# Kernel optimization log

Measured on AMD Instinct MI355X. Metric: run time of the kernel, lower is better.

## Reference

```python
import jax, jax.numpy as jnp
import numpy as np

B, S, DIM = 2, 2048, 2048
H, DK, DR, DC, DCP, DV = 16, 128, 64, 512, 1024, 128


def setup_inputs() -> dict:
    key = jax.random.key(0)
    ks = jax.random.split(key, 8)
    s = 0.02  # weight init scale
    return {
        "x": jax.random.normal(ks[0], (B, S, DIM), jnp.float32),
        "W_c": jax.random.normal(ks[1], (DIM, DC), jnp.float32) * s,
        "W_c_prime": jax.random.normal(ks[2], (DIM, DCP), jnp.float32) * s,
        "W_qc": jax.random.normal(ks[3], (H, DCP, DK), jnp.float32) * s,
        "W_qr": jax.random.normal(ks[4], (H, DCP, DR), jnp.float32) * s,
        "W_kc": jax.random.normal(ks[5], (H, DC, DK), jnp.float32) * s,
        "W_kr": jax.random.normal(ks[6], (DIM, DR), jnp.float32) * s,
        "W_v": jax.random.normal(ks[7], (H, DC, DV), jnp.float32) * s,
    }


def reference(x, W_c, W_c_prime, W_qc, W_qr, W_kc, W_kr, W_v):
    # Latent compressions
    c = x @ W_c                 # [B,S,DC]  compressed KV latent
    cp = x @ W_c_prime          # [B,S,DCP] compressed Q latent
    # Per-head projections, vectorized over heads
    q_c = jnp.einsum('bsc,hck->bhsk', cp, W_qc)   # [B,H,S,DK]
    q_r = jnp.einsum('bsc,hcr->bhsr', cp, W_qr)   # [B,H,S,DR]
    k_c = jnp.einsum('bsc,hck->bhsk', c, W_kc)    # [B,H,S,DK]
    k_r = x @ W_kr                                 # [B,S,DR] shared across heads
    q = jnp.concatenate([q_c, q_r], axis=-1)                               # [B,H,S,DK+DR]
    k = jnp.concatenate([k_c, jnp.broadcast_to(k_r[:, None], (B, H, S, DR))], axis=-1)
    scale = 1.0 / np.sqrt(DK + DR)
    scores = jnp.einsum('bhsd,bhtd->bhst', q, k) * scale                   # [B,H,S,S]
    causal = jnp.tril(jnp.ones((S, S), dtype=bool))
    scores = jnp.where(causal, scores, -jnp.inf)
    probs = jax.nn.softmax(scores.astype(jnp.float32), axis=-1).astype(q.dtype)
    v = jnp.einsum('bsc,hcv->bhsv', c, W_v)                                # [B,H,S,DV]
    out = jnp.einsum('bhst,bhtv->bhsv', probs, v)                          # [B,H,S,DV]
    return out.transpose(0, 2, 1, 3).reshape(B, S, H * DV)                 # concat heads
```

## Files before the change

kernel.cpp:

```cpp
#include <hip/hip_runtime.h>
#include <stdint.h>

typedef __bf16 bf16;
typedef __bf16 bfx8 __attribute__((ext_vector_type(8)));
typedef __bf16 bfx4 __attribute__((ext_vector_type(4)));
typedef float floatx4 __attribute__((ext_vector_type(4)));

#define B_ 2
#define S_ 2048
#define DIM_ 2048
#define H_ 16
#define DK_ 128
#define DR_ 64
#define DC_ 512
#define DCP_ 1024
#define DV_ 128
#define DQK_ 192

#define MASK_VAL (-30000.0f)
#define C1_ 0.10411754f

__global__ void k_prep(
    const float* __restrict__ x, bf16* __restrict__ xb,
    const float* __restrict__ W_c, const float* __restrict__ W_cp,
    const float* __restrict__ W_qc, const float* __restrict__ W_qr,
    const float* __restrict__ W_kc, const float* __restrict__ W_kr,
    const float* __restrict__ W_v,
    bf16* __restrict__ Wt_c, bf16* __restrict__ Wt_cp,
    bf16* __restrict__ Wt_qc, bf16* __restrict__ Wt_qr,
    bf16* __restrict__ Wt_kc, bf16* __restrict__ Wt_kr,
    bf16* __restrict__ Wt_v) {
    __shared__ float tile[32][33];
    int bid0 = blockIdx.x;
    if (bid0 < 4096) {
        size_t i = ((size_t)bid0 * 256 + threadIdx.x) * 8;
        float4 a = *(const float4*)(x + i);
        float4 b = *(const float4*)(x + i + 4);
        bfx8 r;
        r[0] = (bf16)a.x; r[1] = (bf16)a.y; r[2] = (bf16)a.z; r[3] = (bf16)a.w;
        r[4] = (bf16)b.x; r[5] = (bf16)b.y; r[6] = (bf16)b.z; r[7] = (bf16)b.w;
        *(bfx8*)(xb + i) = r;
        return;
    }
    int bid = bid0 - 4096;
    const float* in; bf16* out; int K, N, lx, ly, local;
    if (bid < 1024)      { in = W_c;  out = Wt_c;  K = 2048; N = 512;  lx = 4; ly = 6; local = bid; }
    else if (bid < 3072) { in = W_cp; out = Wt_cp; K = 2048; N = 1024; lx = 5; ly = 6; local = bid - 1024; }
    else if (bid < 5120) { in = W_qc; out = Wt_qc; K = 1024; N = 128;  lx = 2; ly = 5; local = bid - 3072; }
    else if (bid < 6144) { in = W_qr; out = Wt_qr; K = 1024; N = 64;   lx = 1; ly = 5; local = bid - 5120; }
    else if (bid < 7168) { in = W_kc; out = Wt_kc; K = 512;  N = 128;  lx = 2; ly = 4; local = bid - 6144; }
    else if (bid < 7296) { in = W_kr; out = Wt_kr; K = 2048; N = 64;   lx = 1; ly = 6; local = bid - 7168; }
    else                 { in = W_v;  out = Wt_v;  K = 512;  N = 128;  lx = 2; ly = 4; local = bid - 7296; }
    int n0 = (local & ((1 << lx) - 1)) << 5;
    int k0 = ((local >> lx) & ((1 << ly) - 1)) << 5;
    int h  = local >> (lx + ly);
    const float* ip = in + (size_t)h * K * N;
    bf16* op = out + (size_t)h * K * N;
    int tx = threadIdx.x & 31, ty = threadIdx.x >> 5;
#pragma unroll
    for (int i = 0; i < 32; i += 8)
        tile[ty + i][tx] = ip[(size_t)(k0 + ty + i) * N + (n0 + tx)];
    __syncthreads();
#pragma unroll
    for (int i = 0; i < 32; i += 8)
        op[(size_t)(n0 + ty + i) * K + (k0 + tx)] = (bf16)tile[tx][ty + i];
}

__device__ __forceinline__ void gld16(const bf16* g, bf16* l) {
    __builtin_amdgcn_global_load_lds(
        (const __attribute__((address_space(1))) void*)g,
        (__attribute__((address_space(3))) void*)l, 16, 0, 0);
}

__device__ __forceinline__ bfx8 frag_ld(const bf16* lds, int row, int quad) {
    int pb = quad ^ ((row >> 1) & 3);
    return *(const bfx8*)(lds + row * 32 + pb * 8);
}

#define SLICE_ 4096

__device__ __forceinline__ void gemm_core(const bf16* __restrict__ A,
                                          const bf16* __restrict__ Bt,
                                          int K, int rowlimB,
                                          floatx4 acc[4][4],
                                          bf16* A_lds, bf16* B_lds) {
    int tid = threadIdx.x, wave = tid >> 6, lane = tid & 63;
    int l15 = lane & 15, quad = lane >> 4;
    int wm = (wave & 1) * 64, wn = (wave >> 1) * 64;
    int ch0 = wave * 2, ch1 = wave * 2 + 1;
    int r0 = ch0 * 16 + (lane >> 2), r1 = ch1 * 16 + (lane >> 2);
    int kb0 = (lane & 3) ^ ((r0 >> 1) & 3), kb1 = (lane & 3) ^ ((r1 >> 1) & 3);
    int rb0 = r0 <= rowlimB ? r0 : rowlimB;
    int rb1 = r1 <= rowlimB ? r1 : rowlimB;
    const bf16* a0 = A + (size_t)r0 * K + kb0 * 8;
    const bf16* a1 = A + (size_t)r1 * K + kb1 * 8;
    const bf16* b0 = Bt + (size_t)rb0 * K + kb0 * 8;
    const bf16* b1 = Bt + (size_t)rb1 * K + kb1 * 8;
    bf16* da0 = A_lds + ch0 * 512;
    bf16* da1 = A_lds + ch1 * 512;
    bf16* db0 = B_lds + ch0 * 512;
    bf16* db1 = B_lds + ch1 * 512;
    for (int k0 = 0; k0 < K; k0 += 64) {
        __syncthreads();
        gld16(a0 + k0, da0);
        gld16(a1 + k0, da1);
        gld16(b0 + k0, db0);
        gld16(b1 + k0, db1);
        gld16(a0 + k0 + 32, da0 + SLICE_);
        gld16(a1 + k0 + 32, da1 + SLICE_);
        gld16(b0 + k0 + 32, db0 + SLICE_);
        gld16(b1 + k0 + 32, db1 + SLICE_);
        __syncthreads();
#pragma unroll
        for (int sl = 0; sl < 2; ++sl) {
            const bf16* As = A_lds + sl * SLICE_;
            const bf16* Bs = B_lds + sl * SLICE_;
            bfx8 a[4], b[4];
#pragma unroll
            for (int t = 0; t < 4; ++t) a[t] = frag_ld(As, wm + t * 16 + l15, quad);
#pragma unroll
            for (int t = 0; t < 4; ++t) b[t] = frag_ld(Bs, wn + t * 16 + l15, quad);
#pragma unroll
            for (int mt = 0; mt < 4; ++mt)
#pragma unroll
                for (int nt = 0; nt < 4; ++nt)
                    acc[mt][nt] = __builtin_amdgcn_mfma_f32_16x16x32_bf16(
                        a[mt], b[nt], acc[mt][nt], 0, 0, 0);
        }
    }
}

__global__ __launch_bounds__(256, 3) void k_gemm1(
    const bf16* __restrict__ xb, const bf16* __restrict__ Wt_c,
    const bf16* __restrict__ Wt_cp, const bf16* __restrict__ Wt_kr,
    bf16* __restrict__ c_ws, bf16* __restrict__ cp_ws, bf16* __restrict__ kr_ws) {
    __shared__ __attribute__((aligned(16))) bf16 A_lds[2 * SLICE_];
    __shared__ __attribute__((aligned(16))) bf16 B_lds[2 * SLICE_];
    int hw = blockIdx.x + 13 * blockIdx.y;
    int virt = (hw & 7) * 52 + (hw >> 3);
    int bx = virt % 13, by = virt / 13;
    const bf16* Bt; bf16* outp; int ldc, col0, rowlim;
    if (bx < 4)       { Bt = Wt_c  + (size_t)bx * 128 * DIM_;       outp = c_ws;  ldc = DC_;  col0 = bx * 128;       rowlim = 127; }
    else if (bx < 12) { Bt = Wt_cp + (size_t)(bx - 4) * 128 * DIM_; outp = cp_ws; ldc = DCP_; col0 = (bx - 4) * 128; rowlim = 127; }
    else              { Bt = Wt_kr;                                  outp = kr_ws; ldc = DR_;  col0 = 0;              rowlim = 63;  }
    floatx4 acc[4][4];
#pragma unroll
    for (int i = 0; i < 4; ++i)
#pragma unroll
        for (int j = 0; j < 4; ++j) acc[i][j] = (floatx4){0.f, 0.f, 0.f, 0.f};
    gemm_core(xb + (size_t)by * 128 * DIM_, Bt, DIM_, rowlim, acc, A_lds, B_lds);
    int tid = threadIdx.x, wave = tid >> 6, lane = tid & 63;
    int l15 = lane & 15, quad = lane >> 4;
    int wm = (wave & 1) * 64, wn = (wave >> 1) * 64;
#pragma unroll
    for (int mt = 0; mt < 4; ++mt)
#pragma unroll
        for (int nt = 0; nt < 4; ++nt) {
            int n = wn + nt * 16 + l15;
            if (n > rowlim) continue;
#pragma unroll
            for (int r = 0; r < 4; ++r) {
                int m = by * 128 + wm + mt * 16 + quad * 4 + r;
                outp[(size_t)m * ldc + col0 + n] = (bf16)acc[mt][nt][r];
            }
        }
}

__global__ __launch_bounds__(256, 3) void k_gemm23(
    const bf16* __restrict__ cp_ws, const bf16* __restrict__ c_ws,
    const bf16* __restrict__ Wt_qc, const bf16* __restrict__ Wt_qr,
    const bf16* __restrict__ Wt_kc, const bf16* __restrict__ Wt_v,
    bf16* __restrict__ q_ws, bf16* __restrict__ kc_ws, bf16* __restrict__ vt_ws) {
    __shared__ __attribute__((aligned(16))) bf16 A_lds[2 * SLICE_];
    __shared__ __attribute__((aligned(16))) bf16 B_lds[2 * SLICE_];
    int hw = blockIdx.x;
    int c = hw & 7, idx = hw >> 3;
    int tid = threadIdx.x, wave = tid >> 6, lane = tid & 63;
    int l15 = lane & 15, quad = lane >> 4;
    int wm = (wave & 1) * 64, wn = (wave >> 1) * 64;
    floatx4 acc[4][4];
#pragma unroll
    for (int i = 0; i < 4; ++i)
#pragma unroll
        for (int j = 0; j < 4; ++j) acc[i][j] = (floatx4){0.f, 0.f, 0.f, 0.f};
    if (idx < 96) {
        int virt = c * 96 + idx;
        int bx = virt % 3, by = (virt / 3) & 31, hz = c;
        const bf16* Bt;
        if (bx < 2) Bt = Wt_qc + (size_t)(hz * 2 + bx) * DK_ * DCP_;
        else        Bt = Wt_qr + (size_t)hz * 128 * DCP_;
        gemm_core(cp_ws + (size_t)by * 128 * DCP_, Bt, DCP_, 127, acc, A_lds, B_lds);
#pragma unroll
        for (int mt = 0; mt < 4; ++mt)
#pragma unroll
            for (int nt = 0; nt < 4; ++nt) {
                int n = wn + nt * 16 + l15;
                int h, col;
                if (bx < 2) { h = hz * 2 + bx;        col = n; }
                else        { h = hz * 2 + (n >> 6);  col = 128 + (n & 63); }
#pragma unroll
                for (int r = 0; r < 4; ++r) {
                    int m = by * 128 + wm + mt * 16 + quad * 4 + r;
                    int b = m >> 11, s = m & 2047;
                    q_ws[(((size_t)b * H_ + h) * S_ + s) * DQK_ + col] =
                        (bf16)(acc[mt][nt][r] * C1_);
                }
            }
    } else {
        int v2 = c * 128 + (idx - 96);
        int bx = v2 & 1, by = (v2 >> 1) & 31, h = v2 >> 6;
        const bf16* Bt = (bx == 0) ? (Wt_kc + (size_t)h * DK_ * DC_)
                                   : (Wt_v  + (size_t)h * DV_ * DC_);
        gemm_core(c_ws + (size_t)by * 128 * DC_, Bt, DC_, 127, acc, A_lds, B_lds);
#pragma unroll
        for (int mt = 0; mt < 4; ++mt)
#pragma unroll
            for (int nt = 0; nt < 4; ++nt) {
                int n = wn + nt * 16 + l15;
                if (bx == 0) {
#pragma unroll
                    for (int r = 0; r < 4; ++r) {
                        int m = by * 128 + wm + mt * 16 + quad * 4 + r;
                        int b = m >> 11, s = m & 2047;
                        kc_ws[(((size_t)b * H_ + h) * S_ + s) * DK_ + n] = (bf16)acc[mt][nt][r];
                    }
                } else {
                    int m0 = by * 128 + wm + mt * 16 + quad * 4;
                    int b = m0 >> 11, s = m0 & 2047;
                    bfx4 pack;
#pragma unroll
                    for (int r = 0; r < 4; ++r) pack[r] = (bf16)acc[mt][nt][r];
                    *(bfx4*)(&vt_ws[(((size_t)b * H_ + h) * DV_ + n) * S_ + s]) = pack;
                }
            }
    }
}

__global__ __launch_bounds__(256, 2) void k_attn(
    const bf16* __restrict__ q_ws, const bf16* __restrict__ kc_ws,
    const bf16* __restrict__ kr_ws, const bf16* __restrict__ vt_ws,
    float* __restrict__ out) {
    __shared__ __attribute__((aligned(16))) bf16 K_lds[6 * 2048];
    __shared__ __attribute__((aligned(16))) bf16 V_lds[2 * 4096];
    __shared__ __attribute__((aligned(16))) bf16 P_lds[2 * 2048];
    int hw = blockIdx.x + 16 * blockIdx.y;
    int virt = (hw & 7) * 64 + (hw >> 3);
    int p = virt & 15;
    int bh = virt >> 4, b = bh >> 4, h = bh & 15;
    int tid = threadIdx.x, wave = tid >> 6, lane = tid & 63;
    int l15 = lane & 15, quad = lane >> 4;

    bf16 ov = (bf16)(l15 == 0 ? 1.f : 0.f);
    bfx8 ones8 = {ov, ov, ov, ov, ov, ov, ov, ov};

    int rowk = tid >> 2;
    int kb   = (tid & 3) ^ ((tid >> 3) & 3);
    const bf16* kcp[4]; const bf16* krp[2]; const bf16* vp[4];
#pragma unroll
    for (int j = 0; j < 4; ++j)
        kcp[j] = kc_ws + ((size_t)bh * S_ + rowk) * DK_ + j * 32 + kb * 8;
#pragma unroll
    for (int j = 0; j < 2; ++j)
        krp[j] = kr_ws + ((size_t)b * S_ + rowk) * DR_ + j * 32 + kb * 8;
#pragma unroll
    for (int j = 0; j < 4; ++j)
        vp[j] = vt_ws + ((size_t)bh * DV_ + (j & 1) * 64 + rowk) * S_ + (j >> 1) * 32 + kb * 8;
    bf16* kdst = K_lds + (size_t)tid * 8;
    bf16* vdst = V_lds + (size_t)tid * 8;

    for (int ph = 0; ph < 2; ++ph) {
        int qt = ph ? p : 31 - p;
        int q0 = qt * 64, ntiles = qt + 1;

        const bf16* qrow = q_ws + ((size_t)bh * S_ + q0 + wave * 16 + l15) * DQK_;
        bfx8 qf[6];
#pragma unroll
        for (int ks = 0; ks < 6; ++ks)
            qf[ks] = *(const bfx8*)(qrow + ks * 32 + quad * 8);

        floatx4 o_acc[9];
#pragma unroll
        for (int vt = 0; vt < 9; ++vt) o_acc[vt] = (floatx4){0.f, 0.f, 0.f, 0.f};

        bfx8 pk[4], pr[2], pv[4];
#pragma unroll
        for (int j = 0; j < 4; ++j) pk[j] = *(const bfx8*)(kcp[j]);
#pragma unroll
        for (int j = 0; j < 2; ++j) pr[j] = *(const bfx8*)(krp[j]);
#pragma unroll
        for (int j = 0; j < 4; ++j) pv[j] = *(const bfx8*)(vp[j]);

        for (int t = 0; t < ntiles; ++t) {
            __syncthreads();
#pragma unroll
            for (int j = 0; j < 4; ++j) *(bfx8*)(kdst + j * 2048) = pk[j];
#pragma unroll
            for (int j = 0; j < 2; ++j) *(bfx8*)(kdst + (4 + j) * 2048) = pr[j];
#pragma unroll
            for (int j = 0; j < 4; ++j) *(bfx8*)(vdst + j * 2048) = pv[j];
            __syncthreads();
            if (t + 1 < ntiles) {
                size_t kv1 = (size_t)(t + 1) * 64;
#pragma unroll
                for (int j = 0; j < 4; ++j) pk[j] = *(const bfx8*)(kcp[j] + kv1 * DK_);
#pragma unroll
                for (int j = 0; j < 2; ++j) pr[j] = *(const bfx8*)(krp[j] + kv1 * DR_);
#pragma unroll
                for (int j = 0; j < 4; ++j) pv[j] = *(const bfx8*)(vp[j] + kv1);
            }
            floatx4 sc[4];
#pragma unroll
            for (int nt = 0; nt < 4; ++nt) sc[nt] = (floatx4){0.f, 0.f, 0.f, 0.f};
            __builtin_amdgcn_s_setprio(1);
#pragma unroll
            for (int ks = 0; ks < 6; ++ks)
#pragma unroll
                for (int nt = 0; nt < 4; ++nt) {
                    bfx8 kf = frag_ld(K_lds + ks * 2048, nt * 16 + l15, quad);
                    sc[nt] = __builtin_amdgcn_mfma_f32_16x16x32_bf16(qf[ks], kf, sc[nt], 0, 0, 0);
                }
            __builtin_amdgcn_s_setprio(0);
            if (t == ntiles - 1) {
                int kv0 = t * 64;
#pragma unroll
                for (int nt = 0; nt < 4; ++nt)
#pragma unroll
                    for (int r = 0; r < 4; ++r) {
                        int n_g = kv0 + nt * 16 + l15;
                        int q_g = q0 + wave * 16 + quad * 4 + r;
                        if (n_g > q_g) sc[nt][r] = MASK_VAL;
                    }
            }
#pragma unroll
            for (int nt = 0; nt < 4; ++nt)
#pragma unroll
                for (int r = 0; r < 4; ++r) {
                    int prow = wave * 16 + quad * 4 + r;
                    int pcol = nt * 16 + l15;
                    P_lds[(nt >> 1) * 2048 + prow * 32 +
                          ((((pcol >> 3) & 3) ^ ((prow >> 1) & 3)) * 8) + (pcol & 7)] =
                        (bf16)exp2f(sc[nt][r]);
                }
            __builtin_amdgcn_s_setprio(1);
#pragma unroll
            for (int ks2 = 0; ks2 < 2; ++ks2) {
                bfx8 pf = frag_ld(P_lds + ks2 * 2048, wave * 16 + l15, quad);
#pragma unroll
                for (int vt = 0; vt < 8; ++vt) {
                    bfx8 vf = frag_ld(V_lds + ks2 * 4096, vt * 16 + l15, quad);
                    o_acc[vt] = __builtin_amdgcn_mfma_f32_16x16x32_bf16(pf, vf, o_acc[vt], 0, 0, 0);
                }
                o_acc[8] = __builtin_amdgcn_mfma_f32_16x16x32_bf16(pf, ones8, o_acc[8], 0, 0, 0);
            }
            __builtin_amdgcn_s_setprio(0);
        }
        float rinv[4];
#pragma unroll
        for (int r = 0; r < 4; ++r)
            rinv[r] = 1.f / __shfl(o_acc[8][r], lane & 48);
#pragma unroll
        for (int vt = 0; vt < 8; ++vt)
#pragma unroll
            for (int r = 0; r < 4; ++r) {
                int s = q0 + wave * 16 + quad * 4 + r;
                int v = vt * 16 + l15;
                out[((size_t)b * S_ + s) * (H_ * DV_) + h * DV_ + v] = o_acc[vt][r] * rinv[r];
            }
    }
}

extern "C" void kernel_launch(void* const* d_in, const int* in_sizes, int n_in,
                              void* d_out, int out_size, void* d_ws, size_t ws_size,
                              hipStream_t stream) {
    const float* x    = (const float*)d_in[0];
    const float* W_c  = (const float*)d_in[1];
    const float* W_cp = (const float*)d_in[2];
    const float* W_qc = (const float*)d_in[3];
    const float* W_qr = (const float*)d_in[4];
    const float* W_kc = (const float*)d_in[5];
    const float* W_kr = (const float*)d_in[6];
    const float* W_v  = (const float*)d_in[7];
    float* out = (float*)d_out;

    bf16* c_ws  = (bf16*)d_out;
    bf16* cp_ws = c_ws + (size_t)B_ * S_ * DC_;
    bf16* xb    = cp_ws + (size_t)B_ * S_ * DCP_;

    char* ws = (char*)d_ws;
    size_t off = 0;
    auto alloc = [&](size_t elems) { bf16* p = (bf16*)(ws + off); off += elems * sizeof(bf16); return p; };
    bf16* Wt_c  = alloc((size_t)DIM_ * DC_);
    bf16* Wt_cp = alloc((size_t)DIM_ * DCP_);
    bf16* Wt_qc = alloc((size_t)H_ * DCP_ * DK_);
    bf16* Wt_qr = alloc((size_t)H_ * DCP_ * DR_);
    bf16* Wt_kc = alloc((size_t)H_ * DC_ * DK_);
    bf16* Wt_kr = alloc((size_t)DIM_ * DR_);
    bf16* Wt_v  = alloc((size_t)H_ * DC_ * DV_);
    bf16* kr_ws = alloc((size_t)B_ * S_ * DR_);
    bf16* q_ws  = alloc((size_t)B_ * H_ * S_ * DQK_);
    bf16* kc_ws = alloc((size_t)B_ * H_ * S_ * DK_);
    bf16* vt_ws = alloc((size_t)B_ * H_ * DV_ * S_);

    k_prep<<<dim3(12416), 256, 0, stream>>>(
        x, xb, W_c, W_cp, W_qc, W_qr, W_kc, W_kr, W_v,
        Wt_c, Wt_cp, Wt_qc, Wt_qr, Wt_kc, Wt_kr, Wt_v);

    k_gemm1<<<dim3(13, 32), 256, 0, stream>>>(xb, Wt_c, Wt_cp, Wt_kr, c_ws, cp_ws, kr_ws);
    k_gemm23<<<dim3(1792), 256, 0, stream>>>(cp_ws, c_ws, Wt_qc, Wt_qr, Wt_kc, Wt_v,
                                             q_ws, kc_ws, vt_ws);
    k_attn<<<dim3(16, B_ * H_), 256, 0, stream>>>(q_ws, kc_ws, kr_ws, vt_ws, out);
}
```

Measured before the change: 269.4 us.

## Double attention query tile per block and vectorize weight transpose kernel

The attention kernel now processes 128 query rows per block, each wave handling two 16-row tiles, so every K/V tile loaded into LDS feeds twice as many MFMAs. The grid halves to 256 blocks, and launch bounds drop to one block per SM to give room for the doubled accumulators. The aim is to halve K/V global and LDS traffic per output row, at the cost of lower occupancy and fewer blocks to balance across CUs. The weight transpose in the prep kernel is also rewritten to use 64x32 tiles with float4 loads and bf16x4 stores, cutting its block count and instruction overhead.

New measurement: 302.0 us. +12.1%, slower.

```diff
diff --git a/kernel.cpp b/kernel.cpp
--- a/kernel.cpp
+++ b/kernel.cpp
@@ -30,7 +30,7 @@
     bf16* __restrict__ Wt_qc, bf16* __restrict__ Wt_qr,
     bf16* __restrict__ Wt_kc, bf16* __restrict__ Wt_kr,
     bf16* __restrict__ Wt_v) {
-    __shared__ float tile[32][33];
+    __shared__ float tile[64][33];
     int bid0 = blockIdx.x;
     if (bid0 < 4096) {
         size_t i = ((size_t)bid0 * 256 + threadIdx.x) * 8;
@@ -44,26 +44,33 @@
     }
     int bid = bid0 - 4096;
     const float* in; bf16* out; int K, N, lx, ly, local;
-    if (bid < 1024)      { in = W_c;  out = Wt_c;  K = 2048; N = 512;  lx = 4; ly = 6; local = bid; }
-    else if (bid < 3072) { in = W_cp; out = Wt_cp; K = 2048; N = 1024; lx = 5; ly = 6; local = bid - 1024; }
-    else if (bid < 5120) { in = W_qc; out = Wt_qc; K = 1024; N = 128;  lx = 2; ly = 5; local = bid - 3072; }
-    else if (bid < 6144) { in = W_qr; out = Wt_qr; K = 1024; N = 64;   lx = 1; ly = 5; local = bid - 5120; }
-    else if (bid < 7168) { in = W_kc; out = Wt_kc; K = 512;  N = 128;  lx = 2; ly = 4; local = bid - 6144; }
-    else if (bid < 7296) { in = W_kr; out = Wt_kr; K = 2048; N = 64;   lx = 1; ly = 6; local = bid - 7168; }
-    else                 { in = W_v;  out = Wt_v;  K = 512;  N = 128;  lx = 2; ly = 4; local = bid - 7296; }
+    if (bid < 512)       { in = W_c;  out = Wt_c;  K = 2048; N = 512;  lx = 4; ly = 5; local = bid; }
+    else if (bid < 1536) { in = W_cp; out = Wt_cp; K = 2048; N = 1024; lx = 5; ly = 5; local = bid - 512; }
+    else if (bid < 2560) { in = W_qc; out = Wt_qc; K = 1024; N = 128;  lx = 2; ly = 4; local = bid - 1536; }
+    else if (bid < 3072) { in = W_qr; out = Wt_qr; K = 1024; N = 64;   lx = 1; ly = 4; local = bid - 2560; }
+    else if (bid < 3584) { in = W_kc; out = Wt_kc; K = 512;  N = 128;  lx = 2; ly = 3; local = bid - 3072; }
+    else if (bid < 3648) { in = W_kr; out = Wt_kr; K = 2048; N = 64;   lx = 1; ly = 5; local = bid - 3584; }
+    else                 { in = W_v;  out = Wt_v;  K = 512;  N = 128;  lx = 2; ly = 3; local = bid - 3648; }
     int n0 = (local & ((1 << lx) - 1)) << 5;
-    int k0 = ((local >> lx) & ((1 << ly) - 1)) << 5;
+    int k0 = ((local >> lx) & ((1 << ly) - 1)) << 6;
     int h  = local >> (lx + ly);
     const float* ip = in + (size_t)h * K * N;
     bf16* op = out + (size_t)h * K * N;
-    int tx = threadIdx.x & 31, ty = threadIdx.x >> 5;
-#pragma unroll
-    for (int i = 0; i < 32; i += 8)
-        tile[ty + i][tx] = ip[(size_t)(k0 + ty + i) * N + (n0 + tx)];
+    int t = threadIdx.x;
+    int kr = t >> 3, nc = (t & 7) * 4;
+#pragma unroll
+    for (int i = 0; i < 2; ++i)
+        *(float4*)(&tile[kr + i * 32][nc]) =
+            *(const float4*)(ip + (size_t)(k0 + kr + i * 32) * N + n0 + nc);
     __syncthreads();
-#pragma unroll
-    for (int i = 0; i < 32; i += 8)
-        op[(size_t)(n0 + ty + i) * K + (k0 + tx)] = (bf16)tile[tx][ty + i];
+    int nr = t >> 4, kc = (t & 15) * 4;
+#pragma unroll
+    for (int i = 0; i < 2; ++i) {
+        bfx4 w;
+#pragma unroll
+        for (int c = 0; c < 4; ++c) w[c] = (bf16)tile[kc + c][nr + i * 16];
+        *(bfx4*)(op + (size_t)(n0 + nr + i * 16) * K + k0 + kc) = w;
+    }
 }
 
 __device__ __forceinline__ void gld16(const bf16* g, bf16* l) {
@@ -236,17 +243,17 @@
     }
 }
 
-__global__ __launch_bounds__(256, 2) void k_attn(
+__global__ __launch_bounds__(256, 1) void k_attn(
     const bf16* __restrict__ q_ws, const bf16* __restrict__ kc_ws,
     const bf16* __restrict__ kr_ws, const bf16* __restrict__ vt_ws,
     float* __restrict__ out) {
     __shared__ __attribute__((aligned(16))) bf16 K_lds[6 * 2048];
     __shared__ __attribute__((aligned(16))) bf16 V_lds[2 * 4096];
-    __shared__ __attribute__((aligned(16))) bf16 P_lds[2 * 2048];
-    int hw = blockIdx.x + 16 * blockIdx.y;
-    int virt = (hw & 7) * 64 + (hw >> 3);
-    int p = virt & 15;
-    int bh = virt >> 4, b = bh >> 4, h = bh & 15;
+    __shared__ __attribute__((aligned(16))) bf16 P_lds[2 * 4096];
+    int hw = blockIdx.x + 8 * blockIdx.y;
+    int virt = (hw & 7) * 32 + (hw >> 3);
+    int p = virt & 7;
+    int bh = virt >> 3, b = bh >> 4, h = bh & 15;
     int tid = threadIdx.x, wave = tid >> 6, lane = tid & 63;
     int l15 = lane & 15, quad = lane >> 4;
 
@@ -269,18 +276,24 @@
     bf16* vdst = V_lds + (size_t)tid * 8;
 
     for (int ph = 0; ph < 2; ++ph) {
-        int qt = ph ? p : 31 - p;
-        int q0 = qt * 64, ntiles = qt + 1;
-
-        const bf16* qrow = q_ws + ((size_t)bh * S_ + q0 + wave * 16 + l15) * DQK_;
-        bfx8 qf[6];
-#pragma unroll
-        for (int ks = 0; ks < 6; ++ks)
-            qf[ks] = *(const bfx8*)(qrow + ks * 32 + quad * 8);
-
-        floatx4 o_acc[9];
-#pragma unroll
-        for (int vt = 0; vt < 9; ++vt) o_acc[vt] = (floatx4){0.f, 0.f, 0.f, 0.f};
+        int qt = ph ? p : 15 - p;
+        int q0 = qt * 128, ntiles = 2 * qt + 2;
+
+        bfx8 qf[2][6];
+#pragma unroll
+        for (int rt = 0; rt < 2; ++rt) {
+            const bf16* qrow =
+                q_ws + ((size_t)bh * S_ + q0 + wave * 32 + rt * 16 + l15) * DQK_;
+#pragma unroll
+            for (int ks = 0; ks < 6; ++ks)
+                qf[rt][ks] = *(const bfx8*)(qrow + ks * 32 + quad * 8);
+        }
+
+        floatx4 o_acc[2][9];
+#pragma unroll
+        for (int rt = 0; rt < 2; ++rt)
+#pragma unroll
+            for (int vt = 0; vt < 9; ++vt) o_acc[rt][vt] = (floatx4){0.f, 0.f, 0.f, 0.f};
 
         bfx8 pk[4], pr[2], pv[4];
 #pragma unroll
@@ -308,64 +321,78 @@
 #pragma unroll
                 for (int j = 0; j < 4; ++j) pv[j] = *(const bfx8*)(vp[j] + kv1);
             }
-            floatx4 sc[4];
-#pragma unroll
-            for (int nt = 0; nt < 4; ++nt) sc[nt] = (floatx4){0.f, 0.f, 0.f, 0.f};
+            floatx4 sc[2][4];
+#pragma unroll
+            for (int rt = 0; rt < 2; ++rt)
+#pragma unroll
+                for (int nt = 0; nt < 4; ++nt) sc[rt][nt] = (floatx4){0.f, 0.f, 0.f, 0.f};
             __builtin_amdgcn_s_setprio(1);
 #pragma unroll
             for (int ks = 0; ks < 6; ++ks)
 #pragma unroll
                 for (int nt = 0; nt < 4; ++nt) {
                     bfx8 kf = frag_ld(K_lds + ks * 2048, nt * 16 + l15, quad);
-                    sc[nt] = __builtin_amdgcn_mfma_f32_16x16x32_bf16(qf[ks], kf, sc[nt], 0, 0, 0);
+                    sc[0][nt] = __builtin_amdgcn_mfma_f32_16x16x32_bf16(qf[0][ks], kf, sc[0][nt], 0, 0, 0);
+                    sc[1][nt] = __builtin_amdgcn_mfma_f32_16x16x32_bf16(qf[1][ks], kf, sc[1][nt], 0, 0, 0);
                 }
             __builtin_amdgcn_s_setprio(0);
-            if (t == ntiles - 1) {
+            if (t >= ntiles - 2) {
                 int kv0 = t * 64;
 #pragma unroll
+                for (int rt = 0; rt < 2; ++rt)
+#pragma unroll
+                    for (int nt = 0; nt < 4; ++nt)
+#pragma unroll
+                        for (int r = 0; r < 4; ++r) {
+                            int n_g = kv0 + nt * 16 + l15;
+                            int q_g = q0 + wave * 32 + rt * 16 + quad * 4 + r;
+                            if (n_g > q_g) sc[rt][nt][r] = MASK_VAL;
+                        }
+            }
+#pragma unroll
+            for (int rt = 0; rt < 2; ++rt)
+#pragma unroll
                 for (int nt = 0; nt < 4; ++nt)
 #pragma unroll
                     for (int r = 0; r < 4; ++r) {
-                        int n_g = kv0 + nt * 16 + l15;
-                        int q_g = q0 + wave * 16 + quad * 4 + r;
-                        if (n_g > q_g) sc[nt][r] = MASK_VAL;
+                        int prow = wave * 32 + rt * 16 + quad * 4 + r;
+                        int pcol = nt * 16 + l15;
+                        P_lds[(nt >> 1) * 4096 + prow * 32 +
+                              ((((pcol >> 3) & 3) ^ ((prow >> 1) & 3)) * 8) + (pcol & 7)] =
+                            (bf16)exp2f(sc[rt][nt][r]);
                     }
-            }
-#pragma unroll
-            for (int nt = 0; nt < 4; ++nt)
-#pragma unroll
-                for (int r = 0; r < 4; ++r) {
-                    int prow = wave * 16 + quad * 4 + r;
-                    int pcol = nt * 16 + l15;
-                    P_lds[(nt >> 1) * 2048 + prow * 32 +
-                          ((((pcol >> 3) & 3) ^ ((prow >> 1) & 3)) * 8) + (pcol & 7)] =
-                        (bf16)exp2f(sc[nt][r]);
-                }
             __builtin_amdgcn_s_setprio(1);
 #pragma unroll
             for (int ks2 = 0; ks2 < 2; ++ks2) {
-                bfx8 pf = frag_ld(P_lds + ks2 * 2048, wave * 16 + l15, quad);
+                bfx8 pf0 = frag_ld(P_lds + ks2 * 4096, wave * 32 + l15, quad);
+                bfx8 pf1 = frag_ld(P_lds + ks2 * 4096, wave * 32 + 16 + l15, quad);
 #pragma unroll
                 for (int vt = 0; vt < 8; ++vt) {
                     bfx8 vf = frag_ld(V_lds + ks2 * 4096, vt * 16 + l15, quad);
-                    o_acc[vt] = __builtin_amdgcn_mfma_f32_16x16x32_bf16(pf, vf, o_acc[vt], 0, 0, 0);
+                    o_acc[0][vt] = __builtin_amdgcn_mfma_f32_16x16x32_bf16(pf0, vf, o_acc[0][vt], 0, 0, 0);
+                    o_acc[1][vt] = __builtin_amdgcn_mfma_f32_16x16x32_bf16(pf1, vf, o_acc[1][vt], 0, 0, 0);
                 }
-                o_acc[8] = __builtin_amdgcn_mfma_f32_16x16x32_bf16(pf, ones8, o_acc[8], 0, 0, 0);
+                o_acc[0][8] = __builtin_amdgcn_mfma_f32_16x16x32_bf16(pf0, ones8, o_acc[0][8], 0, 0, 0);
+                o_acc[1][8] = __builtin_amdgcn_mfma_f32_16x16x32_bf16(pf1, ones8, o_acc[1][8], 0, 0, 0);
             }
             __builtin_amdgcn_s_setprio(0);
         }
-        float rinv[4];
-#pragma unroll
-        for (int r = 0; r < 4; ++r)
-            rinv[r] = 1.f / __shfl(o_acc[8][r], lane & 48);
-#pragma unroll
-        for (int vt = 0; vt < 8; ++vt)
-#pragma unroll
-            for (int r = 0; r < 4; ++r) {
-                int s = q0 + wave * 16 + quad * 4 + r;
-                int v = vt * 16 + l15;
-                out[((size_t)b * S_ + s) * (H_ * DV_) + h * DV_ + v] = o_acc[vt][r] * rinv[r];
-            }
+#pragma unroll
+        for (int rt = 0; rt < 2; ++rt) {
+            float rinv[4];
+#pragma unroll
+            for (int r = 0; r < 4; ++r)
+                rinv[r] = 1.f / __shfl(o_acc[rt][8][r], lane & 48);
+#pragma unroll
+            for (int vt = 0; vt < 8; ++vt)
+#pragma unroll
+                for (int r = 0; r < 4; ++r) {
+                    int s = q0 + wave * 32 + rt * 16 + quad * 4 + r;
+                    int v = vt * 16 + l15;
+                    out[((size_t)b * S_ + s) * (H_ * DV_) + h * DV_ + v] =
+                        o_acc[rt][vt][r] * rinv[r];
+                }
+        }
     }
 }
 
@@ -401,12 +428,12 @@
     bf16* kc_ws = alloc((size_t)B_ * H_ * S_ * DK_);
     bf16* vt_ws = alloc((size_t)B_ * H_ * DV_ * S_);
 
-    k_prep<<<dim3(12416), 256, 0, stream>>>(
+    k_prep<<<dim3(8256), 256, 0, stream>>>(
         x, xb, W_c, W_cp, W_qc, W_qr, W_kc, W_kr, W_v,
         Wt_c, Wt_cp, Wt_qc, Wt_qr, Wt_kc, Wt_kr, Wt_v);
 
     k_gemm1<<<dim3(13, 32), 256, 0, stream>>>(xb, Wt_c, Wt_cp, Wt_kr, c_ws, cp_ws, kr_ws);
     k_gemm23<<<dim3(1792), 256, 0, stream>>>(cp_ws, c_ws, Wt_qc, Wt_qr, Wt_kc, Wt_v,
                                              q_ws, kc_ws, vt_ws);
-    k_attn<<<dim3(16, B_ * H_), 256, 0, stream>>>(q_ws, kc_ws, kr_ws, vt_ws, out);
-}
+    k_attn<<<dim3(8, B_ * H_), 256, 0, stream>>>(q_ws, kc_ws, kr_ws, vt_ws, out);
+}
```
